# Kernel optimization log

Hardware: AMD Instinct MI355X
Metric: run time of the kernel (lower is better)

## Reference

```python
import jax, jax.numpy as jnp
import numpy as np

B, D1, N, F_IN, F_OUT = 8, 16, 2048, 64, 64


def setup_inputs() -> dict:
    key = jax.random.key(0)
    k1, k2, k3 = jax.random.split(key, 3)
    x = jax.random.normal(k1, (B, D1, N, F_IN), dtype=jnp.float32)
    adj = jax.random.uniform(k2, (B, N, N), dtype=jnp.float32)
    weight = jax.random.normal(k3, (F_IN, F_OUT), dtype=jnp.float32) * (1.0 / np.sqrt(F_IN))
    return {"x": x, "adj": adj, "weight": weight}


def reference(x, adj, weight):
    # x: [B, D1, N, F_in], adj: [B, N, N], weight: [F_in, F_out]
    # Original: per (b, i) loops -> support = x[b,i] @ W; out[b,i] = adj[b] @ support
    # Fused as batched einsums. Note: the module's bias parameter is unused in forward.
    support = jnp.einsum('binf,fg->bing', x, weight)          # feature transform
    out = jnp.einsum('bnm,bimg->bing', adj, support)           # adjacency aggregation
    return out
```

## Files before the change

kernel.cpp:

```cpp
#include <hip/hip_runtime.h>
#include <hip/hip_bf16.h>

typedef __attribute__((ext_vector_type(8))) short bf16x8;
typedef __attribute__((ext_vector_type(4))) float f32x4;

#define NB    8
#define ND1   16
#define NN    2048
#define NF    64
#define GN    1024

__device__ static inline ushort f2bf(float f) {
    unsigned int u = __builtin_bit_cast(unsigned int, f);
    unsigned int r = (u + 0x7FFFu + ((u >> 16) & 1u)) >> 16;
    return (ushort)r;
}

__device__ static inline void gload_lds16(const void* g, void* l) {
    __builtin_amdgcn_global_load_lds(
        (const __attribute__((address_space(1))) void*)g,
        (__attribute__((address_space(3))) void*)l, 16, 0, 0);
}

__global__ __launch_bounds__(256) void conv_adj_kernel(
    const float* __restrict__ adj, ushort* __restrict__ adjb, int n4)
{
    int idx = blockIdx.x * blockDim.x + threadIdx.x;
    int stride = gridDim.x * blockDim.x;
    const float4* a4 = (const float4*)adj;
    ushort4* o4 = (ushort4*)adjb;
    for (int i = idx; i < n4; i += stride) {
        float4 v = a4[i];
        ushort4 r;
        r.x = f2bf(v.x); r.y = f2bf(v.y); r.z = f2bf(v.z); r.w = f2bf(v.w);
        o4[i] = r;
    }
}

__global__ __launch_bounds__(256) void support_kernel(
    const float* __restrict__ x, const float* __restrict__ w,
    ushort* __restrict__ sT)
{
    __shared__ __align__(16) float Ws[64 * 64];
    __shared__ __align__(16) float xs[64 * 65];
    __shared__ __align__(16) ushort tr[64 * 72];

    int t = threadIdx.x;
    int bid = blockIdx.x;
    int b  = bid >> 9;
    int r  = bid & 511;
    int i  = r >> 5;
    int mb = r & 31;

    const float4* w4 = (const float4*)w;
    const float4* x4 = (const float4*)(x + (((size_t)(b * ND1 + i)) * NN + mb * 64) * NF);
#pragma unroll
    for (int j = 0; j < 4; ++j) {
        float4 wv = w4[j * 256 + t];
        int fl = j * 1024 + t * 4;
        Ws[fl + 0] = wv.x; Ws[fl + 1] = wv.y; Ws[fl + 2] = wv.z; Ws[fl + 3] = wv.w;
        float4 xv = x4[j * 256 + t];
        int ml = fl >> 6, f = fl & 63;
        float* xr = &xs[ml * 65 + f];
        xr[0] = xv.x; xr[1] = xv.y; xr[2] = xv.z; xr[3] = xv.w;
    }
    __syncthreads();

    int ml = t & 63;
    int g0 = (t >> 6) * 16;
    f32x4 acc4[4] = {0.f, 0.f, 0.f, 0.f};
    for (int f = 0; f < 64; ++f) {
        float xv = xs[ml * 65 + f];
        const f32x4* wp = (const f32x4*)&Ws[f * 64 + g0];
#pragma unroll
        for (int q = 0; q < 4; ++q) acc4[q] += xv * wp[q];
    }
#pragma unroll
    for (int j = 0; j < 16; ++j)
        tr[(g0 + j) * 72 + ml] = f2bf(acc4[j >> 2][j & 3]);
    __syncthreads();

    int g = t >> 2, part = t & 3;
    const uint4* src = (const uint4*)&tr[g * 72 + part * 16];
    uint4* dst = (uint4*)(sT + ((size_t)(b * GN + i * 64 + g)) * NN + mb * 64 + part * 16);
    dst[0] = src[0];
    dst[1] = src[1];
}

__global__ __launch_bounds__(512, 2) void gemm8_kernel(
    const ushort* __restrict__ adjb,
    const ushort* __restrict__ sT,
    float* __restrict__ out)
{
    __shared__ __align__(16) ushort lds[3 * 16384];

    const int t    = threadIdx.x;
    const int lane = t & 63;
    const int w    = t >> 6;
    const int wm   = w >> 2;
    const int wn   = w & 3;

    int bid  = blockIdx.x;
    int tile = (bid & 7) * 32 + (bid >> 3);
    int b    = tile >> 5;
    int r    = tile & 31;
    int n0   = (r >> 2) * 256;
    int c0   = (r & 3) * 256;

    const ushort* Ab = adjb + (size_t)b * NN * NN + (size_t)n0 * NN;
    const ushort* Bb = sT   + (size_t)b * GN * NN + (size_t)c0 * NN;

    const int rS  = lane & 15;
    const int cgS = lane >> 4;
    const int fq  = ((lane >> 4) * 16 + (lane & 15)) * 8;

    f32x4 acc[8][4];
#pragma unroll
    for (int a = 0; a < 8; ++a)
#pragma unroll
        for (int c = 0; c < 4; ++c) acc[a][c] = (f32x4){0.f, 0.f, 0.f, 0.f};

    auto stageA = [&](int kt, int q) {
#pragma unroll
        for (int j = 0; j < 2; ++j) {
            int stripe = j * 8 + w;
            gload_lds16(Ab + (size_t)(stripe * 16 + rS) * NN + kt * 32 + cgS * 8,
                        &lds[q * 16384 + j * 4096 + w * 512 + lane * 8]);
        }
    };
    auto stageB = [&](int kt, int q) {
#pragma unroll
        for (int j = 0; j < 2; ++j) {
            int stripe = j * 8 + w;
            gload_lds16(Bb + (size_t)(stripe * 16 + rS) * NN + kt * 32 + cgS * 8,
                        &lds[q * 16384 + 8192 + j * 4096 + w * 512 + lane * 8]);
        }
    };

    stageA(0, 0); stageB(0, 0);
    stageA(1, 1); stageB(1, 1);

    int q = 0, qn = 2;
    for (int kt = 0; kt < 64; ++kt) {
        if (kt < 63) asm volatile("s_waitcnt vmcnt(4)" ::: "memory");
        else         asm volatile("s_waitcnt vmcnt(0)" ::: "memory");
        asm volatile("s_barrier" ::: "memory");

        const ushort* La = &lds[q * 16384];
        const ushort* Lb = &lds[q * 16384 + 8192];

        bf16x8 af[4], bfr[4];
#pragma unroll
        for (int a = 0; a < 4; ++a)
            af[a] = *(const bf16x8*)&La[(wm * 8 + a) * 512 + fq];
#pragma unroll
        for (int c = 0; c < 4; ++c)
            bfr[c] = *(const bf16x8*)&Lb[(wn * 4 + c) * 512 + fq];
        if (kt < 62) stageA(kt + 2, qn);
        asm volatile("s_barrier" ::: "memory");
        __builtin_amdgcn_s_setprio(1);
#pragma unroll
        for (int a = 0; a < 4; ++a)
#pragma unroll
            for (int c = 0; c < 4; ++c)
                acc[a][c] = __builtin_amdgcn_mfma_f32_16x16x32_bf16(af[a], bfr[c], acc[a][c], 0, 0, 0);
        __builtin_amdgcn_s_setprio(0);

#pragma unroll
        for (int a = 0; a < 4; ++a)
            af[a] = *(const bf16x8*)&La[(wm * 8 + 4 + a) * 512 + fq];
        if (kt < 62) stageB(kt + 2, qn);
        asm volatile("s_barrier" ::: "memory");
        __builtin_amdgcn_s_setprio(1);
#pragma unroll
        for (int a = 0; a < 4; ++a)
#pragma unroll
            for (int c = 0; c < 4; ++c)
                acc[4 + a][c] = __builtin_amdgcn_mfma_f32_16x16x32_bf16(af[a], bfr[c], acc[4 + a][c], 0, 0, 0);
        __builtin_amdgcn_s_setprio(0);

        q  = (q  == 2) ? 0 : q  + 1;
        qn = (qn == 2) ? 0 : qn + 1;
    }

#pragma unroll
    for (int a = 0; a < 8; ++a) {
        int row0 = n0 + wm * 128 + a * 16 + (lane >> 4) * 4;
#pragma unroll
        for (int c = 0; c < 4; ++c) {
            int col = c0 + wn * 64 + c * 16 + (lane & 15);
            int ii = col >> 6, g = col & 63;
            float* op = out + (((size_t)(b * ND1 + ii)) * NN + row0) * NF + g;
#pragma unroll
            for (int e = 0; e < 4; ++e)
                op[e * NF] = acc[a][c][e];
        }
    }
}

__global__ __launch_bounds__(256) void gcn_gemm_fb_kernel(
    const float* __restrict__ adjf, const ushort* __restrict__ sT,
    float* __restrict__ out)
{
    __shared__ __align__(16) ushort lA[128 * 64];
    __shared__ __align__(16) ushort lB[128 * 64];

    int t = threadIdx.x;
    int bid0 = blockIdx.x;
    int bid = (bid0 & 7) * 128 + (bid0 >> 3);
    int b  = bid >> 7;
    int rr = bid & 127;
    int n0 = (rr >> 3) * 128;
    int c0 = (rr & 7) * 128;

    const float*  Af = adjf + (size_t)b * NN * NN;
    const ushort* Bb = sT + (size_t)b * GN * NN;

    int lane = t & 63, wv = t >> 6;
    int wr = (wv >> 1) * 64, wc = (wv & 1) * 64;

    f32x4 acc[4][4];
#pragma unroll
    for (int a = 0; a < 4; ++a)
#pragma unroll
        for (int c = 0; c < 4; ++c) acc[a][c] = (f32x4){0.f, 0.f, 0.f, 0.f};

    int sRow = t >> 3;
    int sCol = (t & 7) * 8;

    for (int k0 = 0; k0 < NN; k0 += 64) {
#pragma unroll
        for (int i = 0; i < 4; ++i) {
            const float* src = Af + (size_t)(n0 + i * 32 + sRow) * NN + k0 + sCol;
            float4 v0 = *(const float4*)src;
            float4 v1 = *(const float4*)(src + 4);
            union { bf16x8 v; ushort u[8]; } p;
            p.u[0] = f2bf(v0.x); p.u[1] = f2bf(v0.y);
            p.u[2] = f2bf(v0.z); p.u[3] = f2bf(v0.w);
            p.u[4] = f2bf(v1.x); p.u[5] = f2bf(v1.y);
            p.u[6] = f2bf(v1.z); p.u[7] = f2bf(v1.w);
            *(bf16x8*)&lA[(i * 32 + sRow) * 64 + sCol] = p.v;
        }
#pragma unroll
        for (int i = 0; i < 4; ++i)
            gload_lds16(Bb + (size_t)(c0 + i * 32 + sRow) * NN + k0 + sCol,
                        &lB[(i * 32 + sRow) * 64 + sCol]);
        __syncthreads();
#pragma unroll
        for (int kk = 0; kk < 2; ++kk) {
            bf16x8 af[4], bfr[4];
#pragma unroll
            for (int a = 0; a < 4; ++a)
                af[a] = *(const bf16x8*)&lA[(wr + a * 16 + (lane & 15)) * 64 + kk * 32 + (lane >> 4) * 8];
#pragma unroll
            for (int c = 0; c < 4; ++c)
                bfr[c] = *(const bf16x8*)&lB[(wc + c * 16 + (lane & 15)) * 64 + kk * 32 + (lane >> 4) * 8];
#pragma unroll
            for (int a = 0; a < 4; ++a)
#pragma unroll
                for (int c = 0; c < 4; ++c)
                    acc[a][c] = __builtin_amdgcn_mfma_f32_16x16x32_bf16(af[a], bfr[c], acc[a][c], 0, 0, 0);
        }
        __syncthreads();
    }
#pragma unroll
    for (int a = 0; a < 4; ++a) {
        int row0 = n0 + wr + a * 16 + (lane >> 4) * 4;
#pragma unroll
        for (int c = 0; c < 4; ++c) {
            int col = c0 + wc + c * 16 + (lane & 15);
            int ii = col >> 6, g = col & 63;
            float* op = out + (((size_t)(b * ND1 + ii)) * NN + row0) * NF + g;
#pragma unroll
            for (int e = 0; e < 4; ++e)
                op[e * NF] = acc[a][c][e];
        }
    }
}

extern "C" void kernel_launch(void* const* d_in, const int* in_sizes, int n_in,
                              void* d_out, int out_size, void* d_ws, size_t ws_size,
                              hipStream_t stream) {
    const float* x   = (const float*)d_in[0];
    const float* adj = (const float*)d_in[1];
    const float* w   = (const float*)d_in[2];
    float* out = (float*)d_out;

    ushort* sT   = (ushort*)d_ws;
    ushort* adjb = (ushort*)((char*)d_ws + 33554432);
    bool preconv = ws_size >= (size_t)100663296;

    support_kernel<<<dim3(NB * ND1 * (NN / 64)), dim3(256), 0, stream>>>(x, w, sT);

    if (preconv) {
        conv_adj_kernel<<<dim3(2048), dim3(256), 0, stream>>>(adj, adjb, NB * NN * NN / 4);
        gemm8_kernel<<<dim3(256), dim3(512), 0, stream>>>(adjb, sT, out);
    } else {
        gcn_gemm_fb_kernel<<<dim3(NB * 16 * 8), dim3(256), 0, stream>>>(adj, sT, out);
    }
}
```

Before: 341.0 us.

## Merge prep kernels and restage GEMM with 64-wide K double-buffered tiles

Fuses the adjacency bf16 conversion and the support computation into one launch, with block-index ranges choosing the role. This drops a kernel launch and lets the two memory-bound prep phases run concurrently. Converts 8 elements per thread per iteration. Restructures the GEMM main loop to stage 64-wide K tiles into two 64KB-total LDS buffers with explicit vmcnt/lgkmcnt waits and more barriers per tile, which may change occupancy and synchronisation overhead.

```diff
diff --git a/kernel.cpp b/kernel.cpp
--- a/kernel.cpp
+++ b/kernel.cpp
@@ -22,31 +22,38 @@
         (__attribute__((address_space(3))) void*)l, 16, 0, 0);
 }
 
-__global__ __launch_bounds__(256) void conv_adj_kernel(
-    const float* __restrict__ adj, ushort* __restrict__ adjb, int n4)
+__global__ __launch_bounds__(256) void prep_kernel(
+    const float* __restrict__ x, const float* __restrict__ w,
+    const float* __restrict__ adj, ushort* __restrict__ sT,
+    ushort* __restrict__ adjb)
 {
-    int idx = blockIdx.x * blockDim.x + threadIdx.x;
-    int stride = gridDim.x * blockDim.x;
-    const float4* a4 = (const float4*)adj;
-    ushort4* o4 = (ushort4*)adjb;
-    for (int i = idx; i < n4; i += stride) {
-        float4 v = a4[i];
-        ushort4 r;
-        r.x = f2bf(v.x); r.y = f2bf(v.y); r.z = f2bf(v.z); r.w = f2bf(v.w);
-        o4[i] = r;
-    }
-}
-
-__global__ __launch_bounds__(256) void support_kernel(
-    const float* __restrict__ x, const float* __restrict__ w,
-    ushort* __restrict__ sT)
-{
-    __shared__ __align__(16) float Ws[64 * 64];
-    __shared__ __align__(16) float xs[64 * 65];
-    __shared__ __align__(16) ushort tr[64 * 72];
-
+    __shared__ __align__(16) char smem[16384 + 16640];
     int t = threadIdx.x;
-    int bid = blockIdx.x;
+
+    if (blockIdx.x < 2048) {
+        int idx = blockIdx.x * 256 + t;
+        const int stride = 2048 * 256;
+        const float4* a4 = (const float4*)adj;
+        uint4* o4 = (uint4*)adjb;
+        const int n8 = NB * NN * NN / 8;
+        for (int i = idx; i < n8; i += stride) {
+            float4 v0 = a4[2 * i];
+            float4 v1 = a4[2 * i + 1];
+            union { uint4 q; ushort u[8]; } p;
+            p.u[0] = f2bf(v0.x); p.u[1] = f2bf(v0.y);
+            p.u[2] = f2bf(v0.z); p.u[3] = f2bf(v0.w);
+            p.u[4] = f2bf(v1.x); p.u[5] = f2bf(v1.y);
+            p.u[6] = f2bf(v1.z); p.u[7] = f2bf(v1.w);
+            o4[i] = p.q;
+        }
+        return;
+    }
+
+    float*  Ws = (float*)smem;
+    float*  xs = (float*)(smem + 16384);
+    ushort* tr = (ushort*)(smem + 16384);
+
+    int bid = blockIdx.x - 2048;
     int b  = bid >> 9;
     int r  = bid & 511;
     int i  = r >> 5;
@@ -75,6 +82,7 @@
 #pragma unroll
         for (int q = 0; q < 4; ++q) acc4[q] += xv * wp[q];
     }
+    __syncthreads();
 #pragma unroll
     for (int j = 0; j < 16; ++j)
         tr[(g0 + j) * 72 + ml] = f2bf(acc4[j >> 2][j & 3]);
@@ -92,7 +100,7 @@
     const ushort* __restrict__ sT,
     float* __restrict__ out)
 {
-    __shared__ __align__(16) ushort lds[3 * 16384];
+    __shared__ __align__(16) ushort lds[65536];
 
     const int t    = threadIdx.x;
     const int lane = t & 63;
@@ -120,68 +128,73 @@
 #pragma unroll
         for (int c = 0; c < 4; ++c) acc[a][c] = (f32x4){0.f, 0.f, 0.f, 0.f};
 
-    auto stageA = [&](int kt, int q) {
+    auto stg = [&](const ushort* __restrict__ srcb, int tt, int ks, int regionUS) {
 #pragma unroll
         for (int j = 0; j < 2; ++j) {
-            int stripe = j * 8 + w;
-            gload_lds16(Ab + (size_t)(stripe * 16 + rS) * NN + kt * 32 + cgS * 8,
-                        &lds[q * 16384 + j * 4096 + w * 512 + lane * 8]);
+            gload_lds16(srcb + (size_t)((2 * w + j) * 16 + rS) * NN + tt * 64 + ks * 32 + cgS * 8,
+                        &lds[regionUS + (2 * w + j) * 512 + lane * 8]);
         }
     };
-    auto stageB = [&](int kt, int q) {
-#pragma unroll
-        for (int j = 0; j < 2; ++j) {
-            int stripe = j * 8 + w;
-            gload_lds16(Bb + (size_t)(stripe * 16 + rS) * NN + kt * 32 + cgS * 8,
-                        &lds[q * 16384 + 8192 + j * 4096 + w * 512 + lane * 8]);
-        }
-    };
-
-    stageA(0, 0); stageB(0, 0);
-    stageA(1, 1); stageB(1, 1);
-
-    int q = 0, qn = 2;
-    for (int kt = 0; kt < 64; ++kt) {
-        if (kt < 63) asm volatile("s_waitcnt vmcnt(4)" ::: "memory");
-        else         asm volatile("s_waitcnt vmcnt(0)" ::: "memory");
-        asm volatile("s_barrier" ::: "memory");
-
-        const ushort* La = &lds[q * 16384];
-        const ushort* Lb = &lds[q * 16384 + 8192];
-
-        bf16x8 af[4], bfr[4];
-#pragma unroll
-        for (int a = 0; a < 4; ++a)
-            af[a] = *(const bf16x8*)&La[(wm * 8 + a) * 512 + fq];
-#pragma unroll
-        for (int c = 0; c < 4; ++c)
-            bfr[c] = *(const bf16x8*)&Lb[(wn * 4 + c) * 512 + fq];
-        if (kt < 62) stageA(kt + 2, qn);
-        asm volatile("s_barrier" ::: "memory");
-        __builtin_amdgcn_s_setprio(1);
-#pragma unroll
-        for (int a = 0; a < 4; ++a)
-#pragma unroll
-            for (int c = 0; c < 4; ++c)
-                acc[a][c] = __builtin_amdgcn_mfma_f32_16x16x32_bf16(af[a], bfr[c], acc[a][c], 0, 0, 0);
-        __builtin_amdgcn_s_setprio(0);
-
-#pragma unroll
-        for (int a = 0; a < 4; ++a)
-            af[a] = *(const bf16x8*)&La[(wm * 8 + 4 + a) * 512 + fq];
-        if (kt < 62) stageB(kt + 2, qn);
-        asm volatile("s_barrier" ::: "memory");
-        __builtin_amdgcn_s_setprio(1);
-#pragma unroll
-        for (int a = 0; a < 4; ++a)
-#pragma unroll
-            for (int c = 0; c < 4; ++c)
-                acc[4 + a][c] = __builtin_amdgcn_mfma_f32_16x16x32_bf16(af[a], bfr[c], acc[4 + a][c], 0, 0, 0);
-        __builtin_amdgcn_s_setprio(0);
-
-        q  = (q  == 2) ? 0 : q  + 1;
-        qn = (qn == 2) ? 0 : qn + 1;
-    }
+
+#define FRAG_A(Ac_, ksoff, ah)                                                  \
+    _Pragma("unroll")                                                           \
+    for (int a_ = 0; a_ < 4; ++a_)                                              \
+        af[a_] = *(const bf16x8*)&lds[(Ac_) + (ksoff) + (wm * 8 + (ah) * 4 + a_) * 512 + fq];
+#define FRAG_B(Bc_, ksoff)                                                      \
+    _Pragma("unroll")                                                           \
+    for (int c_ = 0; c_ < 4; ++c_)                                              \
+        bfv[c_] = *(const bf16x8*)&lds[(Bc_) + (ksoff) + (wn * 4 + c_) * 512 + fq];
+#define MFMA16(aoff)                                                            \
+    __builtin_amdgcn_s_setprio(1);                                              \
+    _Pragma("unroll")                                                           \
+    for (int a_ = 0; a_ < 4; ++a_)                                              \
+        _Pragma("unroll")                                                       \
+        for (int c_ = 0; c_ < 4; ++c_)                                          \
+            acc[(aoff) + a_][c_] = __builtin_amdgcn_mfma_f32_16x16x32_bf16(     \
+                af[a_], bfv[c_], acc[(aoff) + a_][c_], 0, 0, 0);                \
+    __builtin_amdgcn_s_setprio(0);
+#define BAR() __builtin_amdgcn_s_barrier()
+#define LGKM0() asm volatile("s_waitcnt lgkmcnt(0)" ::: "memory")
+
+#define TILE(tt, S12, S34, W2A, W1A)                                            \
+    {                                                                           \
+        const int buf_ = (tt) & 1;                                              \
+        const int Ac = buf_ * 32768, Bc = Ac + 16384;                           \
+        const int An = (buf_ ^ 1) * 32768, Bn = An + 16384;                     \
+        bf16x8 af[4], bfv[4];                                                   \
+                                                 \
+        FRAG_A(Ac, 0, 0); FRAG_B(Bc, 0);                                        \
+        if (S12) stg(Ab, (tt) + 1, 1, An + 8192);                               \
+        BAR(); LGKM0(); MFMA16(0); BAR();                                       \
+                                               \
+        FRAG_A(Ac, 0, 1);                                                       \
+        if (S12) stg(Bb, (tt) + 1, 1, Bn + 8192);                               \
+        BAR(); LGKM0(); MFMA16(4);                                              \
+        asm volatile(W2A ::: "memory"); BAR();                                  \
+                                                 \
+        FRAG_A(Ac, 8192, 0); FRAG_B(Bc, 8192);                                  \
+        if (S34) stg(Ab, (tt) + 2, 0, Ac);                                      \
+        BAR(); LGKM0(); MFMA16(0); BAR();                                       \
+                                                          \
+        FRAG_A(Ac, 8192, 1);                                                    \
+        if (S34) stg(Bb, (tt) + 2, 0, Bc);                                      \
+        BAR(); LGKM0(); MFMA16(4);                                              \
+        asm volatile(W1A ::: "memory"); BAR();                                  \
+    }
+
+    stg(Ab, 0, 0, 0);
+    stg(Bb, 0, 0, 16384);
+    stg(Ab, 0, 1, 8192);
+    stg(Bb, 0, 1, 24576);
+    stg(Ab, 1, 0, 32768);
+    stg(Bb, 1, 0, 49152);
+    asm volatile("s_waitcnt vmcnt(8)" ::: "memory");
+    BAR();
+
+    for (int tt = 0; tt < 30; ++tt)
+        TILE(tt, 1, 1, "s_waitcnt vmcnt(8)", "s_waitcnt vmcnt(8)");
+    TILE(30, 1, 0, "s_waitcnt vmcnt(8)", "s_waitcnt vmcnt(4)");
+    TILE(31, 0, 0, "s_waitcnt vmcnt(0)", "");
 
 #pragma unroll
     for (int a = 0; a < 8; ++a) {
@@ -196,6 +209,56 @@
                 op[e * NF] = acc[a][c][e];
         }
     }
+}
+
+__global__ __launch_bounds__(256) void support_kernel(
+    const float* __restrict__ x, const float* __restrict__ w,
+    ushort* __restrict__ sT)
+{
+    __shared__ __align__(16) float Ws[64 * 64];
+    __shared__ __align__(16) float xs[64 * 65];
+    __shared__ __align__(16) ushort tr[64 * 72];
+
+    int t = threadIdx.x;
+    int bid = blockIdx.x;
+    int b  = bid >> 9;
+    int r  = bid & 511;
+    int i  = r >> 5;
+    int mb = r & 31;
+
+    const float4* w4 = (const float4*)w;
+    const float4* x4 = (const float4*)(x + (((size_t)(b * ND1 + i)) * NN + mb * 64) * NF);
+#pragma unroll
+    for (int j = 0; j < 4; ++j) {
+        float4 wv = w4[j * 256 + t];
+        int fl = j * 1024 + t * 4;
+        Ws[fl + 0] = wv.x; Ws[fl + 1] = wv.y; Ws[fl + 2] = wv.z; Ws[fl + 3] = wv.w;
+        float4 xv = x4[j * 256 + t];
+        int ml = fl >> 6, f = fl & 63;
+        float* xr = &xs[ml * 65 + f];
+        xr[0] = xv.x; xr[1] = xv.y; xr[2] = xv.z; xr[3] = xv.w;
+    }
+    __syncthreads();
+
+    int ml = t & 63;
+    int g0 = (t >> 6) * 16;
+    f32x4 acc4[4] = {0.f, 0.f, 0.f, 0.f};
+    for (int f = 0; f < 64; ++f) {
+        float xv = xs[ml * 65 + f];
+        const f32x4* wp = (const f32x4*)&Ws[f * 64 + g0];
+#pragma unroll
+        for (int q = 0; q < 4; ++q) acc4[q] += xv * wp[q];
+    }
+#pragma unroll
+    for (int j = 0; j < 16; ++j)
+        tr[(g0 + j) * 72 + ml] = f2bf(acc4[j >> 2][j & 3]);
+    __syncthreads();
+
+    int g = t >> 2, part = t & 3;
+    const uint4* src = (const uint4*)&tr[g * 72 + part * 16];
+    uint4* dst = (uint4*)(sT + ((size_t)(b * GN + i * 64 + g)) * NN + mb * 64 + part * 16);
+    dst[0] = src[0];
+    dst[1] = src[1];
 }
 
 __global__ __launch_bounds__(256) void gcn_gemm_fb_kernel(
@@ -290,12 +353,11 @@
     ushort* adjb = (ushort*)((char*)d_ws + 33554432);
     bool preconv = ws_size >= (size_t)100663296;
 
-    support_kernel<<<dim3(NB * ND1 * (NN / 64)), dim3(256), 0, stream>>>(x, w, sT);
-
     if (preconv) {
-        conv_adj_kernel<<<dim3(2048), dim3(256), 0, stream>>>(adj, adjb, NB * NN * NN / 4);
+        prep_kernel<<<dim3(6144), dim3(256), 0, stream>>>(x, w, adj, sT, adjb);
         gemm8_kernel<<<dim3(256), dim3(512), 0, stream>>>(adjb, sT, out);
     } else {
+        support_kernel<<<dim3(NB * ND1 * (NN / 64)), dim3(256), 0, stream>>>(x, w, sT);
         gcn_gemm_fb_kernel<<<dim3(NB * 16 * 8), dim3(256), 0, stream>>>(adj, sT, out);
     }
 }
```

Result: slower. 354.5 us (+4.0%).
